# Performance work log

Hardware: AMD Instinct MI355X
Metric: run time of the kernel (lower is better)

## Reference

```python
import jax, jax.numpy as jnp
import numpy as np
import math

V, T, D, N, H, DFF = 32000, 1024, 1024, 6, 16, 4096
DK = D // H
EPS = 1e-6


def setup_inputs() -> dict:
    key = jax.random.key(0)
    ks = jax.random.split(key, 20)
    s = 0.02
    B = 2
    return {
        "idx": jax.random.randint(ks[0], (B, T), 0, V, dtype=jnp.int32),
        "emb": jax.random.normal(ks[1], (V, D), jnp.float32) * s,
        # attention projections, stored [in, out] so y = x @ W
        "Wq": jax.random.normal(ks[2], (N, D, D), jnp.float32) * s,
        "Wk": jax.random.normal(ks[3], (N, D, D), jnp.float32) * s,
        "Wv": jax.random.normal(ks[4], (N, D, D), jnp.float32) * s,
        "Wo": jax.random.normal(ks[5], (N, D, D), jnp.float32) * s,
        "ln1_a": jnp.ones((N, D), jnp.float32),
        "ln1_b": jnp.zeros((N, D), jnp.float32),
        "ln2_a": jnp.ones((N, D), jnp.float32),
        "ln2_b": jnp.zeros((N, D), jnp.float32),
        "W1": jax.random.normal(ks[6], (N, D, DFF), jnp.float32) * s,
        "b1": jnp.zeros((N, DFF), jnp.float32),
        "W2": jax.random.normal(ks[7], (N, DFF, D), jnp.float32) * s,
        "b2": jnp.zeros((N, D), jnp.float32),
        "fnorm_a": jnp.ones((D,), jnp.float32),
        "fnorm_b": jnp.zeros((D,), jnp.float32),
        "Wp": jax.random.normal(ks[8], (D, V), jnp.float32) * s,
        "bp": jnp.zeros((V,), jnp.float32),
    }


def _layernorm(x, a, b):
    # torch .std() uses Bessel correction (ddof=1); denom is (std + eps), not sqrt(var+eps)
    mean = x.mean(axis=-1, keepdims=True)
    std = jnp.std(x, axis=-1, keepdims=True, ddof=1)
    return a * (x - mean) / (std + EPS) + b


def _pos_encoding(t, d):
    pos = jnp.arange(t, dtype=jnp.float32)[:, None]
    div = jnp.exp(jnp.arange(0, d, 2, dtype=jnp.float32) * (-math.log(10000.0) / d))
    pe = jnp.zeros((t, d), jnp.float32)
    pe = pe.at[:, 0::2].set(jnp.sin(pos * div))
    pe = pe.at[:, 1::2].set(jnp.cos(pos * div))
    return pe


def _forward(idx, emb, Wq, Wk, Wv, Wo, ln1_a, ln1_b, ln2_a, ln2_b,
             W1, b1, W2, b2, fnorm_a, fnorm_b, Wp, bp):
    B, Tc = idx.shape
    x = emb[idx] * math.sqrt(D) + _pos_encoding(Tc, D)  # [B,T,D]
    causal = jnp.tril(jnp.ones((Tc, Tc), bool))  # [T,T]

    def block(x, p):
        wq, wk, wv, wo, a1, c1, a2, c2, w1, bb1, w2, bb2 = p
        h_in = _layernorm(x, a1, c1)
        q = (h_in @ wq).reshape(B, Tc, H, DK).transpose(0, 2, 1, 3)
        k = (h_in @ wk).reshape(B, Tc, H, DK).transpose(0, 2, 1, 3)
        v = (h_in @ wv).reshape(B, Tc, H, DK).transpose(0, 2, 1, 3)
        scores = jnp.einsum('bhqd,bhkd->bhqk', q, k) / math.sqrt(DK)
        scores = jnp.where(causal, scores, -1e9)
        attn = jax.nn.softmax(scores, axis=-1)
        o = jnp.einsum('bhqk,bhkd->bhqd', attn, v)
        o = o.transpose(0, 2, 1, 3).reshape(B, Tc, D) @ wo
        x = x + o
        h2 = _layernorm(x, a2, c2)
        ff = jax.nn.relu(h2 @ w1 + bb1) @ w2 + bb2
        x = x + ff
        return x, None

    x, _ = jax.lax.scan(block, x, (Wq, Wk, Wv, Wo, ln1_a, ln1_b, ln2_a, ln2_b, W1, b1, W2, b2))
    x = _layernorm(x, fnorm_a, fnorm_b)
    logits = x @ Wp + bp  # [B,T,V]
    return logits


def reference(idx, emb, Wq, Wk, Wv, Wo, ln1_a, ln1_b, ln2_a, ln2_b,
              W1, b1, W2, b2, fnorm_a, fnorm_b, Wp, bp):
    return _forward(idx, emb, Wq, Wk, Wv, Wo, ln1_a, ln1_b, ln2_a, ln2_b,
                    W1, b1, W2, b2, fnorm_a, fnorm_b, Wp, bp)
```

## Files before the change

### kernel.cpp

```cpp
#include <hip/hip_runtime.h>
#include <hip/hip_bf16.h>
#include <math.h>

#define VOCAB 32000
#define TSEQ 1024
#define DMODEL 1024
#define NLAYERS 6
#define NHEADS 16
#define DFF 4096
#define DKH 64
#define BATCH 2
#define MROWS (BATCH * TSEQ)
#define LN_EPS 1e-6f
#define QKVS 3072

typedef unsigned short u16;
typedef __attribute__((ext_vector_type(8))) short short8v;
typedef __attribute__((ext_vector_type(4))) float f32x4;

__device__ __forceinline__ u16 f2bb(float f) {
    __hip_bfloat16 h = __float2bfloat16(f);
    u16 u; __builtin_memcpy(&u, &h, 2); return u;
}

__device__ __forceinline__ void gload16(const void* g, void* l) {
    __builtin_amdgcn_global_load_lds(
        (const __attribute__((address_space(1))) unsigned int*)g,
        (__attribute__((address_space(3))) unsigned int*)l, 16, 0, 0);
}

__global__ void embed_kernel(const int* __restrict__ idx,
                             const float* __restrict__ emb,
                             float* __restrict__ x) {
    int i = blockIdx.x * blockDim.x + threadIdx.x;
    if (i >= MROWS * DMODEL) return;
    int row = i / DMODEL;
    int d = i - row * DMODEL;
    int t = row % TSEQ;
    int tok = idx[row];
    float e = emb[(size_t)tok * DMODEL + d] * 32.0f;
    float freq = expf(-(float)(d & ~1) * (9.210340371976184f / (float)DMODEL));
    float ang = (float)t * freq;
    float pe = (d & 1) ? cosf(ang) : sinf(ang);
    x[i] = e + pe;
}

template<bool OB16>
__global__ void __launch_bounds__(256) ln_kernel(const float* __restrict__ x,
                                                 const float* __restrict__ a,
                                                 const float* __restrict__ b,
                                                 void* __restrict__ yv) {
    __shared__ float red[8];
    int row = blockIdx.x;
    int tid = threadIdx.x;
    float4 v = ((const float4*)(x + (size_t)row * DMODEL))[tid];
    float s = v.x + v.y + v.z + v.w;
    #pragma unroll
    for (int off = 32; off; off >>= 1) s += __shfl_xor(s, off, 64);
    if ((tid & 63) == 0) red[tid >> 6] = s;
    __syncthreads();
    float mean = (red[0] + red[1] + red[2] + red[3]) * (1.0f / DMODEL);
    float dx = v.x - mean, dy = v.y - mean, dz = v.z - mean, dw = v.w - mean;
    float ss = dx * dx + dy * dy + dz * dz + dw * dw;
    #pragma unroll
    for (int off = 32; off; off >>= 1) ss += __shfl_xor(ss, off, 64);
    if ((tid & 63) == 0) red[4 + (tid >> 6)] = ss;
    __syncthreads();
    float var = (red[4] + red[5] + red[6] + red[7]) * (1.0f / (DMODEL - 1));
    float inv = 1.0f / (sqrtf(var) + LN_EPS);
    const float4 a4 = ((const float4*)a)[tid];
    const float4 b4 = ((const float4*)b)[tid];
    float o0 = a4.x * dx * inv + b4.x;
    float o1 = a4.y * dy * inv + b4.y;
    float o2 = a4.z * dz * inv + b4.z;
    float o3 = a4.w * dw * inv + b4.w;
    if (OB16) {
        ushort4 o; o.x = f2bb(o0); o.y = f2bb(o1); o.z = f2bb(o2); o.w = f2bb(o3);
        ((ushort4*)((u16*)yv + (size_t)row * DMODEL))[tid] = o;
    } else {
        float4 o; o.x = o0; o.y = o1; o.z = o2; o.w = o3;
        ((float4*)((float*)yv + (size_t)row * DMODEL))[tid] = o;
    }
}

__global__ void __launch_bounds__(256) convT(const float* __restrict__ in,
                                             u16* __restrict__ out, int K, int N) {
    __shared__ float t[32][33];
    in  += (size_t)blockIdx.z * K * N;
    out += (size_t)blockIdx.z * K * N;
    const int tx = threadIdx.x, ty = threadIdx.y;
    const int n0 = blockIdx.x * 32, k0 = blockIdx.y * 32;
    #pragma unroll
    for (int i = 0; i < 4; ++i)
        t[ty + i * 8][tx] = in[(size_t)(k0 + ty + i * 8) * N + n0 + tx];
    __syncthreads();
    #pragma unroll
    for (int i = 0; i < 4; ++i)
        out[(size_t)(n0 + ty + i * 8) * K + k0 + tx] = f2bb(t[tx][ty + i * 8]);
}

__global__ void __launch_bounds__(256) convQKVO(const float* __restrict__ Wq,
                                                const float* __restrict__ Wk,
                                                const float* __restrict__ Wv,
                                                const float* __restrict__ Wo,
                                                u16* __restrict__ WqkvT,
                                                u16* __restrict__ WoT) {
    __shared__ float t[32][33];
    const int z = blockIdx.z, L = z >> 2, p = z & 3;
    const size_t MM = (size_t)DMODEL * DMODEL;
    const float* in = (p == 0 ? Wq : p == 1 ? Wk : p == 2 ? Wv : Wo) + (size_t)L * MM;
    u16* out = (p < 3) ? (WqkvT + (size_t)L * 3 * MM + (size_t)p * MM)
                       : (WoT + (size_t)L * MM);
    const int tx = threadIdx.x, ty = threadIdx.y;
    const int n0 = blockIdx.x * 32, k0 = blockIdx.y * 32;
    #pragma unroll
    for (int i = 0; i < 4; ++i)
        t[ty + i * 8][tx] = in[(size_t)(k0 + ty + i * 8) * DMODEL + n0 + tx];
    __syncthreads();
    #pragma unroll
    for (int i = 0; i < 4; ++i)
        out[(size_t)(n0 + ty + i * 8) * DMODEL + k0 + tx] = f2bb(t[tx][ty + i * 8]);
}

template<int BMT, bool BIAS, bool RELU, bool RES, bool OB16>
__global__ void __launch_bounds__(256) gemm_mfma(
    const u16* __restrict__ A, const u16* __restrict__ Bt,
    const float* __restrict__ bias, const float* res,
    void* outp, int N, int K)
{
    constexpr int MR = BMT / 32;
    constexpr int AR = BMT / 64;
    __shared__ u16 Alds[2][BMT * 32];
    __shared__ u16 Blds[2][128 * 32];
    const int tid = threadIdx.x;
    const int w = tid >> 6, lane = tid & 63;
    const int wr = w >> 1, wc = w & 1;
    const size_t bm = (size_t)blockIdx.y * BMT;
    const size_t bn = (size_t)blockIdx.x * 128;
    const int srow = (w << 4) + (lane >> 2);
    const int scol = (((lane & 3) ^ ((lane >> 3) & 3)) << 3);
    const int fr = lane & 15, fq = lane >> 4;
    const int aswz = ((fq ^ ((fr >> 1) & 3)) << 3);

    f32x4 acc[MR][4];
    #pragma unroll
    for (int m = 0; m < MR; ++m)
        #pragma unroll
        for (int n = 0; n < 4; ++n)
            acc[m][n] = (f32x4){0.f, 0.f, 0.f, 0.f};

    #pragma unroll
    for (int li = 0; li < AR; ++li)
        gload16(A + (bm + li * 64 + srow) * K + scol, Alds[0] + li * 2048 + w * 512);
    #pragma unroll
    for (int li = 0; li < 2; ++li)
        gload16(Bt + (bn + li * 64 + srow) * K + scol, Blds[0] + li * 2048 + w * 512);
    __syncthreads();

    int cur = 0;
    for (int k0 = 0; k0 < K; k0 += 32) {
        if (k0 + 32 < K) {
            const int nb = cur ^ 1;
            #pragma unroll
            for (int li = 0; li < AR; ++li)
                gload16(A + (bm + li * 64 + srow) * K + k0 + 32 + scol, Alds[nb] + li * 2048 + w * 512);
            #pragma unroll
            for (int li = 0; li < 2; ++li)
                gload16(Bt + (bn + li * 64 + srow) * K + k0 + 32 + scol, Blds[nb] + li * 2048 + w * 512);
        }
        short8v a[MR], b[4];
        #pragma unroll
        for (int m = 0; m < MR; ++m)
            a[m] = *(const short8v*)(Alds[cur] + (wr * (BMT / 2) + m * 16 + fr) * 32 + aswz);
        #pragma unroll
        for (int n = 0; n < 4; ++n)
            b[n] = *(const short8v*)(Blds[cur] + (wc * 64 + n * 16 + fr) * 32 + aswz);
        #pragma unroll
        for (int m = 0; m < MR; ++m)
            #pragma unroll
            for (int n = 0; n < 4; ++n)
                acc[m][n] = __builtin_amdgcn_mfma_f32_16x16x32_bf16(a[m], b[n], acc[m][n], 0, 0, 0);
        __syncthreads();
        cur ^= 1;
    }

    #pragma unroll
    for (int n = 0; n < 4; ++n) {
        const size_t col = bn + wc * 64 + n * 16 + fr;
        const float bv = BIAS ? bias[col] : 0.f;
        #pragma unroll
        for (int m = 0; m < MR; ++m) {
            #pragma unroll
            for (int r = 0; r < 4; ++r) {
                const size_t row = bm + wr * (BMT / 2) + m * 16 + fq * 4 + r;
                float v = acc[m][n][r] + bv;
                if (RELU) v = fmaxf(v, 0.f);
                if (RES)  v += res[row * N + col];
                if (OB16) ((u16*)outp)[row * N + col] = f2bb(v);
                else      ((float*)outp)[row * N + col] = v;
            }
        }
    }
}

__global__ void __launch_bounds__(256) attn_flash(const u16* __restrict__ qkv,
                                                  u16* __restrict__ o) {
    __shared__ u16 Klds[64 * 64];
    __shared__ u16 Vt[64 * 64];
    __shared__ u16 Plds[4][16 * 72];

    const int tid = threadIdx.x;
    const int w = tid >> 6, lane = tid & 63;
    const int fr = lane & 15, fq = lane >> 4;
    const int qt = gridDim.x - 1 - blockIdx.x;
    const int h = blockIdx.y, b = blockIdx.z;
    const int qbase = qt * 64 + w * 16;
    const size_t rowbase = (size_t)b * TSEQ;
    const int hd = h * DKH;

    const u16* qrow = qkv + (rowbase + qbase + fr) * QKVS + hd;
    const short8v qf0 = *(const short8v*)(qrow + fq * 8);
    const short8v qf1 = *(const short8v*)(qrow + 32 + fq * 8);

    float m[4], l[4];
    f32x4 oa[4];
    #pragma unroll
    for (int r = 0; r < 4; ++r) { m[r] = -1e30f; l[r] = 0.f; }
    #pragma unroll
    for (int nd = 0; nd < 4; ++nd) oa[nd] = (f32x4){0.f, 0.f, 0.f, 0.f};

    for (int t = 0; t <= qt; ++t) {
        const int j0 = t * 64;
        #pragma unroll
        for (int half = 0; half < 2; ++half) {
            const int r = (tid >> 3) + half * 32;
            const int c8 = (tid & 7) << 3;
            const size_t grow = (rowbase + j0 + r) * QKVS + hd + c8;
            short8v kv = *(const short8v*)(qkv + grow + 1024);
            int kbyte = (r * 128 + c8 * 2) ^ ((r & 7) << 4);
            *(short8v*)((char*)Klds + kbyte) = kv;
            short8v vv = *(const short8v*)(qkv + grow + 2048);
            #pragma unroll
            for (int i = 0; i < 8; ++i) {
                const int vrow = c8 + i;
                const int slot = ((r >> 3) + (vrow >> 3)) & 7;
                Vt[vrow * 64 + slot * 8 + (r & 7)] = (u16)vv[i];
            }
        }
        __syncthreads();

        f32x4 s[4];
        __builtin_amdgcn_s_setprio(1);
        #pragma unroll
        for (int ct = 0; ct < 4; ++ct) {
            const int krow = ct * 16 + fr;
            const int swz = (krow & 7) << 4;
            short8v k0 = *(const short8v*)((char*)Klds + ((krow * 128 + fq * 16) ^ swz));
            short8v k1 = *(const short8v*)((char*)Klds + ((krow * 128 + 64 + fq * 16) ^ swz));
            f32x4 a = (f32x4){0.f, 0.f, 0.f, 0.f};
            a = __builtin_amdgcn_mfma_f32_16x16x32_bf16(qf0, k0, a, 0, 0, 0);
            a = __builtin_amdgcn_mfma_f32_16x16x32_bf16(qf1, k1, a, 0, 0, 0);
            s[ct] = a;
        }
        __builtin_amdgcn_s_setprio(0);

        float c[4];
        #pragma unroll
        for (int r = 0; r < 4; ++r) {
            const int qg = qbase + fq * 4 + r;
            float sv[4];
            #pragma unroll
            for (int ct = 0; ct < 4; ++ct) {
                sv[ct] = s[ct][r] * 0.125f;
                if (j0 + ct * 16 + fr > qg) sv[ct] = -1e30f;
            }
            float mx = fmaxf(fmaxf(sv[0], sv[1]), fmaxf(sv[2], sv[3]));
            mx = fmaxf(mx, __shfl_xor(mx, 1, 64));
            mx = fmaxf(mx, __shfl_xor(mx, 2, 64));
            mx = fmaxf(mx, __shfl_xor(mx, 4, 64));
            mx = fmaxf(mx, __shfl_xor(mx, 8, 64));
            const float mn = fmaxf(m[r], mx);
            c[r] = __expf(m[r] - mn);
            m[r] = mn;
            float p0 = __expf(sv[0] - mn);
            float p1 = __expf(sv[1] - mn);
            float p2 = __expf(sv[2] - mn);
            float p3 = __expf(sv[3] - mn);
            float rs = (p0 + p1) + (p2 + p3);
            rs += __shfl_xor(rs, 1, 64);
            rs += __shfl_xor(rs, 2, 64);
            rs += __shfl_xor(rs, 4, 64);
            rs += __shfl_xor(rs, 8, 64);
            l[r] = l[r] * c[r] + rs;
            u16* prow = &Plds[w][(fq * 4 + r) * 72];
            prow[fr]      = f2bb(p0);
            prow[16 + fr] = f2bb(p1);
            prow[32 + fr] = f2bb(p2);
            prow[48 + fr] = f2bb(p3);
        }
        #pragma unroll
        for (int nd = 0; nd < 4; ++nd)
            #pragma unroll
            for (int r = 0; r < 4; ++r)
                oa[nd][r] *= c[r];
        asm volatile("s_waitcnt lgkmcnt(0)" ::: "memory");
        __builtin_amdgcn_sched_barrier(0);

        __builtin_amdgcn_s_setprio(1);
        #pragma unroll
        for (int ks = 0; ks < 2; ++ks) {
            const short8v pf = *(const short8v*)(&Plds[w][fr * 72 + ks * 32 + fq * 8]);
            #pragma unroll
            for (int nd = 0; nd < 4; ++nd) {
                const int vrow = nd * 16 + fr;
                const int slot = (ks * 4 + fq + (vrow >> 3)) & 7;
                const short8v vf = *(const short8v*)(&Vt[vrow * 64 + slot * 8]);
                oa[nd] = __builtin_amdgcn_mfma_f32_16x16x32_bf16(pf, vf, oa[nd], 0, 0, 0);
            }
        }
        __builtin_amdgcn_s_setprio(0);
        __syncthreads();
    }

    #pragma unroll
    for (int r = 0; r < 4; ++r) {
        const float inv = 1.0f / l[r];
        u16* orow = o + (rowbase + qbase + fq * 4 + r) * DMODEL + hd;
        #pragma unroll
        for (int nd = 0; nd < 4; ++nd)
            orow[nd * 16 + fr] = f2bb(oa[nd][r] * inv);
    }
}

#define FBM 64
#define FBN 64
#define FBK 16
__global__ void __launch_bounds__(256) gemm_f32(
    const float* __restrict__ A, const float* __restrict__ Bw,
    const float* __restrict__ bias, float* outp, int N, int K)
{
    __shared__ float As[FBK][FBM];
    __shared__ float Bs[FBK][FBN];
    const int bm = blockIdx.y * FBM, bn = blockIdx.x * FBN;
    const int tid = threadIdx.x;
    const int tr = (tid >> 4) << 2, tc = (tid & 15) << 2;
    const int am = tid >> 2, ak = (tid & 3) << 2;
    const int bk = tid >> 4, bn4 = (tid & 15) << 2;
    float acc[4][4] = {};
    const float* Ap = A + (size_t)(bm + am) * K + ak;
    const float* Bp = Bw + (size_t)bk * N + bn + bn4;
    for (int k0 = 0; k0 < K; k0 += FBK) {
        float4 av = *(const float4*)(Ap + k0);
        float4 bv = *(const float4*)(Bp + (size_t)k0 * N);
        As[ak + 0][am] = av.x; As[ak + 1][am] = av.y; As[ak + 2][am] = av.z; As[ak + 3][am] = av.w;
        *(float4*)&Bs[bk][bn4] = bv;
        __syncthreads();
        #pragma unroll
        for (int kk = 0; kk < FBK; ++kk) {
            float4 a4 = *(const float4*)&As[kk][tr];
            float4 b4 = *(const float4*)&Bs[kk][tc];
            acc[0][0] += a4.x*b4.x; acc[0][1] += a4.x*b4.y; acc[0][2] += a4.x*b4.z; acc[0][3] += a4.x*b4.w;
            acc[1][0] += a4.y*b4.x; acc[1][1] += a4.y*b4.y; acc[1][2] += a4.y*b4.z; acc[1][3] += a4.y*b4.w;
            acc[2][0] += a4.z*b4.x; acc[2][1] += a4.z*b4.y; acc[2][2] += a4.z*b4.z; acc[2][3] += a4.z*b4.w;
            acc[3][0] += a4.w*b4.x; acc[3][1] += a4.w*b4.y; acc[3][2] += a4.w*b4.z; acc[3][3] += a4.w*b4.w;
        }
        __syncthreads();
    }
    #pragma unroll
    for (int i = 0; i < 4; ++i) {
        int row = bm + tr + i;
        float4 o;
        o.x = acc[i][0] + bias[bn + tc + 0];
        o.y = acc[i][1] + bias[bn + tc + 1];
        o.z = acc[i][2] + bias[bn + tc + 2];
        o.w = acc[i][3] + bias[bn + tc + 3];
        *(float4*)(outp + (size_t)row * N + bn + tc) = o;
    }
}

extern "C" void kernel_launch(void* const* d_in, const int* in_sizes, int n_in,
                              void* d_out, int out_size, void* d_ws, size_t ws_size,
                              hipStream_t stream) {
    const int* idx = (const int*)d_in[0];
    const float* emb = (const float*)d_in[1];
    const float* Wq = (const float*)d_in[2];
    const float* Wk = (const float*)d_in[3];
    const float* Wv = (const float*)d_in[4];
    const float* Wo = (const float*)d_in[5];
    const float* ln1a = (const float*)d_in[6];
    const float* ln1b = (const float*)d_in[7];
    const float* ln2a = (const float*)d_in[8];
    const float* ln2b = (const float*)d_in[9];
    const float* W1 = (const float*)d_in[10];
    const float* b1 = (const float*)d_in[11];
    const float* W2 = (const float*)d_in[12];
    const float* b2 = (const float*)d_in[13];
    const float* fa = (const float*)d_in[14];
    const float* fb = (const float*)d_in[15];
    const float* Wp = (const float*)d_in[16];
    const float* bp = (const float*)d_in[17];
    float* out = (float*)d_out;

    const size_t MD = (size_t)MROWS * DMODEL;
    const size_t MM = (size_t)DMODEL * DMODEL;
    u16* U = (u16*)out;
    u16* qkv = U;
    u16* ob = U + 3 * MD;
    u16* hb = U + 4 * MD;
    float* x = (float*)(U + 5 * MD);
    u16* ff = U + 7 * MD;
    u16* WqkvT = U + 12 * MD;
    u16* WoT = U + 21 * MD;
    u16* W1T = U + 24 * MD;
    u16* W2T = U + 36 * MD;

    const bool pathA = ws_size >= (size_t)68 * 1024 * 1024 + 256;
    u16* WpT = (u16*)d_ws;
    u16* h2b = (u16*)((char*)d_ws + (size_t)64 * 1024 * 1024);
    float* hF = (float*)d_ws;

    dim3 cblk(32, 8);
    convQKVO<<<dim3(32, 32, 24), cblk, 0, stream>>>(Wq, Wk, Wv, Wo, WqkvT, WoT);
    convT<<<dim3(128, 32, 6), cblk, 0, stream>>>(W1, W1T, DMODEL, DFF);
    convT<<<dim3(32, 128, 6), cblk, 0, stream>>>(W2, W2T, DFF, DMODEL);
    if (pathA) convT<<<dim3(1000, 32, 1), cblk, 0, stream>>>(Wp, WpT, DMODEL, VOCAB);

    embed_kernel<<<(MROWS * DMODEL + 255) / 256, 256, 0, stream>>>(idx, emb, x);

    for (int L = 0; L < NLAYERS; ++L) {
        ln_kernel<true><<<MROWS, 256, 0, stream>>>(x, ln1a + (size_t)L * DMODEL, ln1b + (size_t)L * DMODEL, hb);
        gemm_mfma<128, false, false, false, true><<<dim3(24, 16), 256, 0, stream>>>(
            hb, WqkvT + (size_t)L * 3 * MM, nullptr, nullptr, qkv, QKVS, DMODEL);
        attn_flash<<<dim3(TSEQ / 64, NHEADS, BATCH), 256, 0, stream>>>(qkv, ob);
        gemm_mfma<64, false, false, true, false><<<dim3(8, 32), 256, 0, stream>>>(
            ob, WoT + (size_t)L * MM, nullptr, x, x, DMODEL, DMODEL);
        ln_kernel<true><<<MROWS, 256, 0, stream>>>(x, ln2a + (size_t)L * DMODEL, ln2b + (size_t)L * DMODEL, hb);
        gemm_mfma<128, true, true, false, true><<<dim3(32, 16), 256, 0, stream>>>(
            hb, W1T + (size_t)L * DFF * DMODEL, b1 + (size_t)L * DFF, nullptr, ff, DFF, DMODEL);
        gemm_mfma<64, true, false, true, false><<<dim3(8, 32), 256, 0, stream>>>(
            ff, W2T + (size_t)L * DFF * DMODEL, b2 + (size_t)L * DMODEL, x, x, DMODEL, DFF);
    }

    if (pathA) {
        ln_kernel<true><<<MROWS, 256, 0, stream>>>(x, fa, fb, h2b);
        gemm_mfma<128, true, false, false, false><<<dim3(250, 16), 256, 0, stream>>>(
            h2b, WpT, bp, nullptr, out, VOCAB, DMODEL);
    } else {
        ln_kernel<false><<<MROWS, 256, 0, stream>>>(x, fa, fb, hF);
        gemm_f32<<<dim3(VOCAB / FBN, MROWS / FBM), 256, 0, stream>>>(hF, Wp, bp, out, VOCAB, DMODEL);
    }
}
```

Before: 1.706 ms.

## Prefetch next K/V tile into registers and pack V transpose stores

The flash attention loop now issues global loads for the next K/V tile into registers before computing the current tile, using two alternating register sets, so global memory latency overlaps with the MFMA work. The V-transpose staging is reorganized so each thread handles two adjacent key rows and writes 32-bit packed pairs to LDS instead of 16-bit scalar stores. This raises register pressure, which may reduce occupancy.

```diff
diff --git a/kernel.cpp b/kernel.cpp
--- a/kernel.cpp
+++ b/kernel.cpp
@@ -218,6 +218,9 @@
     const size_t rowbase = (size_t)b * TSEQ;
     const int hd = h * DKH;
 
+    const int rk = tid >> 3;
+    const int c8 = (tid & 7) << 3;
+
     const u16* qrow = qkv + (rowbase + qbase + fr) * QKVS + hd;
     const short8v qf0 = *(const short8v*)(qrow + fq * 8);
     const short8v qf1 = *(const short8v*)(qrow + 32 + fq * 8);
@@ -229,26 +232,35 @@
     #pragma unroll
     for (int nd = 0; nd < 4; ++nd) oa[nd] = (f32x4){0.f, 0.f, 0.f, 0.f};
 
-    for (int t = 0; t <= qt; ++t) {
+    short8v ka0, ka1, va0, va1;
+    short8v kb0, kb1, vb0, vb1;
+
+    auto load_set = [&](int j0, short8v& k0v, short8v& k1v, short8v& v0v, short8v& v1v) {
+        const size_t gk = (rowbase + j0 + rk) * QKVS + hd + c8 + 1024;
+        k0v = *(const short8v*)(qkv + gk);
+        k1v = *(const short8v*)(qkv + gk + (size_t)32 * QKVS);
+        const size_t gv = (rowbase + j0 + 2 * rk) * QKVS + hd + c8 + 2048;
+        v0v = *(const short8v*)(qkv + gv);
+        v1v = *(const short8v*)(qkv + gv + QKVS);
+    };
+    auto stage_set = [&](const short8v& k0v, const short8v& k1v,
+                         const short8v& v0v, const short8v& v1v) {
+        const int kb0b = (rk * 128 + c8 * 2) ^ ((rk & 7) << 4);
+        *(short8v*)((char*)Klds + kb0b) = k0v;
+        const int r2 = rk + 32;
+        const int kb1b = (r2 * 128 + c8 * 2) ^ ((r2 & 7) << 4);
+        *(short8v*)((char*)Klds + kb1b) = k1v;
+        #pragma unroll
+        for (int i = 0; i < 8; ++i) {
+            const int vrow = c8 + i;
+            const int slot = (((2 * rk) >> 3) + (vrow >> 3)) & 7;
+            unsigned int pair = ((unsigned int)(u16)v0v[i]) |
+                                (((unsigned int)(u16)v1v[i]) << 16);
+            *(unsigned int*)(&Vt[vrow * 64 + slot * 8 + ((2 * rk) & 7)]) = pair;
+        }
+    };
+    auto do_tile = [&](int t) {
         const int j0 = t * 64;
-        #pragma unroll
-        for (int half = 0; half < 2; ++half) {
-            const int r = (tid >> 3) + half * 32;
-            const int c8 = (tid & 7) << 3;
-            const size_t grow = (rowbase + j0 + r) * QKVS + hd + c8;
-            short8v kv = *(const short8v*)(qkv + grow + 1024);
-            int kbyte = (r * 128 + c8 * 2) ^ ((r & 7) << 4);
-            *(short8v*)((char*)Klds + kbyte) = kv;
-            short8v vv = *(const short8v*)(qkv + grow + 2048);
-            #pragma unroll
-            for (int i = 0; i < 8; ++i) {
-                const int vrow = c8 + i;
-                const int slot = ((r >> 3) + (vrow >> 3)) & 7;
-                Vt[vrow * 64 + slot * 8 + (r & 7)] = (u16)vv[i];
-            }
-        }
-        __syncthreads();
-
         f32x4 s[4];
         __builtin_amdgcn_s_setprio(1);
         #pragma unroll
@@ -319,7 +331,23 @@
             }
         }
         __builtin_amdgcn_s_setprio(0);
-        __syncthreads();
+    };
+
+    load_set(0, ka0, ka1, va0, va1);
+    int t = 0;
+    for (;;) {
+        stage_set(ka0, ka1, va0, va1);
+        __syncthreads();
+        if (t < qt) load_set((t + 1) * 64, kb0, kb1, vb0, vb1);
+        do_tile(t);
+        __syncthreads();
+        if (++t > qt) break;
+        stage_set(kb0, kb1, vb0, vb1);
+        __syncthreads();
+        if (t < qt) load_set((t + 1) * 64, ka0, ka1, va0, va1);
+        do_tile(t);
+        __syncthreads();
+        if (++t > qt) break;
     }
 
     #pragma unroll
```

Measured after the change: 1.676 ms. Within noise of the previous version (-1.8%).
